# Performance work log

Measured on AMD Instinct MI355X. Metric: run time of the kernel, lower is better.

The kernel has to match this reference:

```python
import jax, jax.numpy as jnp
import numpy as np
import math

N_HEADS = 8
D_EMBED = 512
D_CROSS = 768
FF_DIM = 2048
D_HEAD = D_EMBED // N_HEADS


def _gelu_tanh(x):
    # matches the module's hand-written tanh GELU
    return 0.5 * x * (1.0 + jnp.tanh(jnp.sqrt(2.0 / jnp.pi) * (x + 0.044715 * x ** 3)))


def _layer_norm(x, g, b, eps=1e-5):
    mu = jnp.mean(x, axis=-1, keepdims=True)
    var = jnp.var(x, axis=-1, keepdims=True)
    return (x - mu) * jax.lax.rsqrt(var + eps) * g + b


def setup_inputs() -> dict:
    key = jax.random.key(0)
    ks = jax.random.split(key, 20)
    s = 0.02
    inp = {
        "x": jax.random.normal(ks[0], (2, 4096, D_EMBED), jnp.float32),
        "y": jax.random.normal(ks[1], (2, 77, D_CROSS), jnp.float32),
        # self-attention: fused in_proj [D, 3D]
        "sa_in_w": jax.random.normal(ks[2], (D_EMBED, 3 * D_EMBED), jnp.float32) * s,
        "sa_in_b": jnp.zeros((3 * D_EMBED,), jnp.float32),
        "sa_out_w": jax.random.normal(ks[3], (D_EMBED, D_EMBED), jnp.float32) * s,
        "sa_out_b": jnp.zeros((D_EMBED,), jnp.float32),
        # cross-attention
        "ca_q_w": jax.random.normal(ks[4], (D_EMBED, D_EMBED), jnp.float32) * s,
        "ca_q_b": jnp.zeros((D_EMBED,), jnp.float32),
        "ca_k_w": jax.random.normal(ks[5], (D_CROSS, D_EMBED), jnp.float32) * s,
        "ca_k_b": jnp.zeros((D_EMBED,), jnp.float32),
        "ca_v_w": jax.random.normal(ks[6], (D_CROSS, D_EMBED), jnp.float32) * s,
        "ca_v_b": jnp.zeros((D_EMBED,), jnp.float32),
        "ca_out_w": jax.random.normal(ks[7], (D_EMBED, D_EMBED), jnp.float32) * s,
        "ca_out_b": jnp.zeros((D_EMBED,), jnp.float32),
        # feed-forward
        "ff_w1": jax.random.normal(ks[8], (D_EMBED, FF_DIM), jnp.float32) * s,
        "ff_b1": jnp.zeros((FF_DIM,), jnp.float32),
        "ff_w2": jax.random.normal(ks[9], (FF_DIM, D_EMBED), jnp.float32) * s,
        "ff_b2": jnp.zeros((D_EMBED,), jnp.float32),
        # layer norms
        "ln1_g": jnp.ones((D_EMBED,), jnp.float32),
        "ln1_b": jnp.zeros((D_EMBED,), jnp.float32),
        "ln2_g": jnp.ones((D_EMBED,), jnp.float32),
        "ln2_b": jnp.zeros((D_EMBED,), jnp.float32),
        "ln3_g": jnp.ones((D_EMBED,), jnp.float32),
        "ln3_b": jnp.zeros((D_EMBED,), jnp.float32),
    }
    return inp


def _mha(q, k, v):
    # q,k,v: [B, S, D] -> split heads -> attention -> merge
    B, Sq, D = q.shape
    Skv = k.shape[1]
    qh = q.reshape(B, Sq, N_HEADS, D_HEAD).transpose(0, 2, 1, 3)
    kh = k.reshape(B, Skv, N_HEADS, D_HEAD).transpose(0, 2, 1, 3)
    vh = v.reshape(B, Skv, N_HEADS, D_HEAD).transpose(0, 2, 1, 3)
    scores = jnp.einsum("bhqd,bhkd->bhqk", qh, kh) / math.sqrt(D_HEAD)
    w = jax.nn.softmax(scores, axis=-1)
    out = jnp.einsum("bhqk,bhkd->bhqd", w, vh)
    return out.transpose(0, 2, 1, 3).reshape(B, Sq, D)


def reference(x, y, sa_in_w, sa_in_b, sa_out_w, sa_out_b,
              ca_q_w, ca_q_b, ca_k_w, ca_k_b, ca_v_w, ca_v_b, ca_out_w, ca_out_b,
              ff_w1, ff_b1, ff_w2, ff_b2,
              ln1_g, ln1_b, ln2_g, ln2_b, ln3_g, ln3_b):
    # self-attention (no causal mask; default causal_mask=False)
    qkv = x @ sa_in_w + sa_in_b
    q, k, v = jnp.split(qkv, 3, axis=-1)
    sa = _mha(q, k, v) @ sa_out_w + sa_out_b
    x = _layer_norm(x + sa, ln1_g, ln1_b)

    # cross-attention to y
    qc = x @ ca_q_w + ca_q_b
    kc = y @ ca_k_w + ca_k_b
    vc = y @ ca_v_w + ca_v_b
    ca = _mha(qc, kc, vc) @ ca_out_w + ca_out_b
    x = _layer_norm(x + ca, ln2_g, ln2_b)

    # feed-forward with tanh GELU
    ff = _gelu_tanh(x @ ff_w1 + ff_b1) @ ff_w2 + ff_b2
    x = _layer_norm(x + ff, ln3_g, ln3_b)
    return x
```

## Files before the change

kernel.cpp:

```cpp
#include <hip/hip_runtime.h>
#include <stdint.h>

typedef float floatx4 __attribute__((ext_vector_type(4)));
typedef __bf16 bf16x8 __attribute__((ext_vector_type(8)));
typedef unsigned int uintx4 __attribute__((ext_vector_type(4)));
typedef unsigned short ushort_t;

__device__ __forceinline__ float b2f(ushort_t u) {
  union { unsigned int i; float f; } x; x.i = ((unsigned int)u) << 16; return x.f;
}
__device__ __forceinline__ ushort_t f2b(float f) {
  union { float f; unsigned int i; } x; x.f = f;
  unsigned int i = x.i;
  return (ushort_t)((i + 0x7FFFu + ((i >> 16) & 1u)) >> 16);
}
__device__ __forceinline__ unsigned fbits(float f) {
  union { float f; unsigned u; } x; x.f = f; return x.u;
}
__device__ __forceinline__ uintx4 ld16(const void* p) {
  uintx4 v; __builtin_memcpy(&v, p, 16); return v;
}
__device__ __forceinline__ void st16(void* p, uintx4 v) { __builtin_memcpy(p, &v, 16); }
__device__ __forceinline__ floatx4 f4splat(float x) { floatx4 v = {x, x, x, x}; return v; }
__device__ __forceinline__ void sched_fence() { asm volatile("" ::: "memory"); }

__device__ __forceinline__ floatx4 mfma16(uintx4 a, uintx4 b, floatx4 c) {
  return __builtin_amdgcn_mfma_f32_16x16x32_bf16(
      __builtin_bit_cast(bf16x8, a), __builtin_bit_cast(bf16x8, b), c, 0, 0, 0);
}

__device__ __forceinline__ void gll16(const ushort_t* g, ushort_t* l) {
  __builtin_amdgcn_global_load_lds(
      (__attribute__((address_space(1))) void*)(g),
      (__attribute__((address_space(3))) void*)(l), 16, 0, 0);
}

template <int EPI, int NT>
__global__ __launch_bounds__(256, 2) void gemm_bt(
    const ushort_t* __restrict__ A, const ushort_t* __restrict__ Bt,
    const float* __restrict__ bias, void* __restrict__ Cout,
    int N, int K) {
  constexpr int NI = NT / 32;
  __shared__ alignas(16) ushort_t lA[128 * 32];
  __shared__ alignas(16) ushort_t lB[NT * 32];
  const int tid = threadIdx.x;
  const int wave = tid >> 6, lane = tid & 63;
  const int quad = lane >> 4, l16 = lane & 15;
  const int bm = blockIdx.y * 128, bn = blockIdx.x * NT;
  const int wm = (wave >> 1) * 64, wn = (wave & 1) * (NT / 2);

  const ushort_t* ag0 = A + (size_t)(bm + wave * 32 + (lane >> 2)) * K + (lane & 3) * 8;
  const ushort_t* ag1 = ag0 + (size_t)16 * K;
  ushort_t* la = lA + wave * 1024;
  const ushort_t* bg0;
  const ushort_t* bg1 = nullptr;
  ushort_t* lb;
  if (NT == 128) {
    bg0 = Bt + (size_t)(bn + wave * 32 + (lane >> 2)) * K + (lane & 3) * 8;
    bg1 = bg0 + (size_t)16 * K;
    lb = lB + wave * 1024;
  } else {
    bg0 = Bt + (size_t)(bn + wave * 16 + (lane >> 2)) * K + (lane & 3) * 8;
    lb = lB + wave * 512;
  }

  floatx4 acc[4][NI];
#pragma unroll
  for (int i = 0; i < 4; i++)
#pragma unroll
    for (int j = 0; j < NI; j++) acc[i][j] = f4splat(0.f);

  for (int k0 = 0; k0 < K; k0 += 32) {
    __syncthreads();
    gll16(ag0 + k0, la);
    gll16(ag1 + k0, la + 512);
    gll16(bg0 + k0, lb);
    if (NT == 128) gll16(bg1 + k0, lb + 512);
    __syncthreads();
    uintx4 af[4], bf[NI];
#pragma unroll
    for (int i = 0; i < 4; i++) af[i] = ld16(&lA[(wm + i * 16 + l16) * 32 + quad * 8]);
#pragma unroll
    for (int i = 0; i < NI; i++) bf[i] = ld16(&lB[(wn + i * 16 + l16) * 32 + quad * 8]);
#pragma unroll
    for (int mi = 0; mi < 4; mi++)
#pragma unroll
      for (int ni = 0; ni < NI; ni++) acc[mi][ni] = mfma16(af[mi], bf[ni], acc[mi][ni]);
  }

  float bv[NI];
#pragma unroll
  for (int ni = 0; ni < NI; ni++) bv[ni] = bias[bn + wn + ni * 16 + l16];

#pragma unroll
  for (int mi = 0; mi < 4; mi++)
#pragma unroll
    for (int ni = 0; ni < NI; ni++)
#pragma unroll
      for (int r = 0; r < 4; r++) {
        int row = bm + wm + mi * 16 + quad * 4 + r;
        int col = bn + wn + ni * 16 + l16;
        float v = acc[mi][ni][r] + bv[ni];
        if (EPI == 2) {
          float w = v + 0.044715f * v * v * v;
          float e = __builtin_amdgcn_exp2f(-2.3022084f * w);
          v = v * __builtin_amdgcn_rcpf(1.f + e);
        }
        if (EPI == 1)
          ((float*)Cout)[(size_t)row * N + col] = v;
        else
          ((ushort_t*)Cout)[(size_t)row * N + col] = f2b(v);
      }
}

__global__ __launch_bounds__(256) void pack_k(const ushort_t* __restrict__ qkv,
                                              ushort_t* __restrict__ KP) {
  int g = blockIdx.x * 256 + threadIdx.x;
  int lane = g & 63;
  int frag = (g >> 6) & 7;
  int kt = (g >> 9) & 63;
  int bh = g >> 15;
  int b = bh >> 3, h = bh & 7;
  int ni = frag >> 1, kf = frag & 1;
  int l16 = lane & 15, quad = lane >> 4;
  const ushort_t* src = qkv + (size_t)(b * 4096 + kt * 64 + ni * 16 + l16) * 1536 +
                        512 + h * 64 + kf * 32 + quad * 8;
  st16(KP + (size_t)g * 8, ld16(src));
}

__global__ __launch_bounds__(256) void pack_v(const ushort_t* __restrict__ qkv,
                                              ushort_t* __restrict__ VP) {
  __shared__ ushort_t t[64 * 72];
  int bh = blockIdx.x, kt = blockIdx.y;
  int b = bh >> 3, h = bh & 7;
  int tid = threadIdx.x;
#pragma unroll
  for (int i = 0; i < 2; i++) {
    int c = i * 256 + tid;
    int row = c >> 3, c8 = (c & 7) * 8;
    uintx4 d4 = ld16(qkv + (size_t)(b * 4096 + kt * 64 + row) * 1536 + 1024 + h * 64 + c8);
    ushort_t tmp[8];
    __builtin_memcpy(tmp, &d4, 16);
#pragma unroll
    for (int j = 0; j < 8; j++) t[(c8 + j) * 72 + row] = tmp[j];
  }
  __syncthreads();
#pragma unroll
  for (int i = 0; i < 2; i++) {
    int c = i * 256 + tid;
    int frag = c >> 6, lane = c & 63;
    int f = frag >> 2, dn = frag & 3;
    int l16 = lane & 15, quad = lane >> 4;
    uintx4 d4 = ld16(&t[(dn * 16 + l16) * 72 + f * 32 + quad * 8]);
    st16(VP + ((size_t)(bh * 64 + kt) * 8 + frag) * 512 + (size_t)lane * 8, d4);
  }
}

__global__ __launch_bounds__(256, 2) void flash_self(
    const ushort_t* __restrict__ qkv, const ushort_t* __restrict__ KP,
    const ushort_t* __restrict__ VP, ushort_t* __restrict__ outp) {
  __shared__ alignas(16) ushort_t lPT[4 * 32 * 72];
  const int tid = threadIdx.x, wave = tid >> 6, lane = tid & 63;
  const int quad = lane >> 4, l16 = lane & 15;
  const int bh = blockIdx.x, b = bh >> 3, h = bh & 7;
  const int qt = blockIdx.y;

  const ushort_t* Qb = qkv + (size_t)b * 4096 * 1536 + h * 64;
  const ushort_t* KPb = KP + (size_t)bh * 64 * 4096;
  const ushort_t* VPb = VP + (size_t)bh * 64 * 4096;

  uintx4 qf[2][2];
#pragma unroll
  for (int mi = 0; mi < 2; mi++)
#pragma unroll
    for (int kf = 0; kf < 2; kf++)
      qf[mi][kf] = ld16(Qb + (size_t)(qt * 128 + wave * 32 + mi * 16 + l16) * 1536 +
                        kf * 32 + quad * 8);

  floatx4 O[2][4];
#pragma unroll
  for (int mi = 0; mi < 2; mi++)
#pragma unroll
    for (int dn = 0; dn < 4; dn++) O[mi][dn] = f4splat(0.f);
  float lsum[2] = {0.f, 0.f};
  const float c = 0.18033688f;
  ushort_t* PTw = lPT + wave * 32 * 72;

#pragma unroll 2
  for (int kt = 0; kt < 64; kt++) {
    const ushort_t* kb = KPb + kt * 4096;
    uintx4 kfr[4][2];
#pragma unroll
    for (int ni = 0; ni < 4; ni++)
#pragma unroll
      for (int kf = 0; kf < 2; kf++)
        kfr[ni][kf] = ld16(kb + ((ni * 2 + kf) * 64 + lane) * 8);

    floatx4 S[2][4];
#pragma unroll
    for (int ni = 0; ni < 4; ni++)
#pragma unroll
      for (int mi = 0; mi < 2; mi++) {
        floatx4 z = f4splat(0.f);
        z = mfma16(kfr[ni][0], qf[mi][0], z);
        z = mfma16(kfr[ni][1], qf[mi][1], z);
        S[mi][ni] = z;
      }

    const ushort_t* vbp = VPb + kt * 4096;
    uintx4 vf[2][4];
#pragma unroll
    for (int f = 0; f < 2; f++)
#pragma unroll
      for (int dn = 0; dn < 4; dn++)
        vf[f][dn] = ld16(vbp + ((f * 4 + dn) * 64 + lane) * 8);

#pragma unroll
    for (int mi = 0; mi < 2; mi++) {
      float rs = 0.f;
#pragma unroll
      for (int ni = 0; ni < 4; ni++) {
        float p0 = __builtin_amdgcn_exp2f(S[mi][ni][0] * c);
        float p1 = __builtin_amdgcn_exp2f(S[mi][ni][1] * c);
        float p2 = __builtin_amdgcn_exp2f(S[mi][ni][2] * c);
        float p3 = __builtin_amdgcn_exp2f(S[mi][ni][3] * c);
        rs += (p0 + p1) + (p2 + p3);
        unsigned dd[2];
        dd[0] = (fbits(p1) & 0xFFFF0000u) | (fbits(p0) >> 16);
        dd[1] = (fbits(p3) & 0xFFFF0000u) | (fbits(p2) >> 16);
        __builtin_memcpy(&PTw[(mi * 16 + l16) * 72 + ni * 16 + quad * 4], dd, 8);
      }
      lsum[mi] += rs;
    }
    sched_fence();

#pragma unroll
    for (int f = 0; f < 2; f++) {
      uintx4 pf0 = ld16(&PTw[(0 + l16) * 72 + f * 32 + quad * 8]);
      uintx4 pf1 = ld16(&PTw[(16 + l16) * 72 + f * 32 + quad * 8]);
#pragma unroll
      for (int dn = 0; dn < 4; dn++) {
        O[0][dn] = mfma16(vf[f][dn], pf0, O[0][dn]);
        O[1][dn] = mfma16(vf[f][dn], pf1, O[1][dn]);
      }
    }
  }

#pragma unroll
  for (int mi = 0; mi < 2; mi++) {
    lsum[mi] += __shfl_xor(lsum[mi], 16);
    lsum[mi] += __shfl_xor(lsum[mi], 32);
  }

#pragma unroll
  for (int mi = 0; mi < 2; mi++) {
    float inv = 1.0f / lsum[mi];
    const size_t rowg = (size_t)b * 4096 + qt * 128 + wave * 32 + mi * 16 + l16;
#pragma unroll
    for (int dn = 0; dn < 4; dn++) {
      unsigned u0 = (unsigned)f2b(O[mi][dn][0] * inv) | ((unsigned)f2b(O[mi][dn][1] * inv) << 16);
      unsigned u1 = (unsigned)f2b(O[mi][dn][2] * inv) | ((unsigned)f2b(O[mi][dn][3] * inv) << 16);
      unsigned uu[2] = {u0, u1};
      __builtin_memcpy(outp + rowg * 512 + h * 64 + dn * 16 + quad * 4, uu, 8);
    }
  }
}

__global__ __launch_bounds__(256, 2) void cross_attn(
    const ushort_t* __restrict__ qc, const ushort_t* __restrict__ kc,
    const ushort_t* __restrict__ vc, ushort_t* __restrict__ outp) {
  __shared__ alignas(16) ushort_t lK[96 * 72];
  __shared__ alignas(16) ushort_t lV[64 * 104];
  __shared__ alignas(16) ushort_t lP[128 * 104];
  const int tid = threadIdx.x, wave = tid >> 6, lane = tid & 63;
  const int quad = lane >> 4, l16 = lane & 15;
  const int bh = blockIdx.y, b = bh >> 3, h = bh & 7;
  const int qt = blockIdx.x;

#pragma unroll
  for (int i = 0; i < 3; i++) {
    int ch = i * 256 + tid;
    int r = ch >> 3, c8 = ch & 7;
    uintx4 d = {0u, 0u, 0u, 0u};
    if (r < 77) d = ld16(kc + (size_t)(b * 77 + r) * 512 + h * 64 + c8 * 8);
    st16(&lK[r * 72 + c8 * 8], d);
  }
  for (int i = 0; i < 24; i++) {
    int e = i * 256 + tid;
    int dd = e / 96, s = e - dd * 96;
    ushort_t v = 0;
    if (s < 77) v = vc[(size_t)(b * 77 + s) * 512 + h * 64 + dd];
    lV[dd * 104 + s] = v;
  }
  __syncthreads();

  const int qr0 = qt * 128 + wave * 32;
  uintx4 qf[2][2];
#pragma unroll
  for (int mi = 0; mi < 2; mi++)
#pragma unroll
    for (int kf = 0; kf < 2; kf++)
      qf[mi][kf] =
          ld16(qc + (size_t)(b * 4096 + qr0 + mi * 16 + l16) * 512 + h * 64 + kf * 32 + quad * 8);

  floatx4 S[2][6];
#pragma unroll
  for (int ni = 0; ni < 6; ni++) {
    uintx4 k0 = ld16(&lK[(ni * 16 + l16) * 72 + quad * 8]);
    uintx4 k1 = ld16(&lK[(ni * 16 + l16) * 72 + 32 + quad * 8]);
#pragma unroll
    for (int mi = 0; mi < 2; mi++) {
      floatx4 z = f4splat(0.f);
      z = mfma16(qf[mi][0], k0, z);
      z = mfma16(qf[mi][1], k1, z);
      S[mi][ni] = z;
    }
  }
  const float c = 0.18033688f;
#pragma unroll
  for (int ni = 4; ni < 6; ni++)
    if (ni * 16 + l16 >= 77) {
      S[0][ni] = f4splat(-1e30f);
      S[1][ni] = f4splat(-1e30f);
    }

  floatx4 linv[2];
#pragma unroll
  for (int mi = 0; mi < 2; mi++) {
    floatx4 cm = S[mi][0];
#pragma unroll
    for (int ni = 1; ni < 6; ni++)
#pragma unroll
      for (int r = 0; r < 4; r++) cm[r] = fmaxf(cm[r], S[mi][ni][r]);
#pragma unroll
    for (int off = 1; off < 16; off <<= 1)
#pragma unroll
      for (int r = 0; r < 4; r++) cm[r] = fmaxf(cm[r], __shfl_xor(cm[r], off));
    floatx4 rs = f4splat(0.f);
#pragma unroll
    for (int ni = 0; ni < 6; ni++)
#pragma unroll
      for (int r = 0; r < 4; r++) {
        float p = __builtin_amdgcn_exp2f(S[mi][ni][r] * c - cm[r] * c);
        S[mi][ni][r] = p;
        rs[r] += p;
      }
#pragma unroll
    for (int off = 1; off < 16; off <<= 1)
#pragma unroll
      for (int r = 0; r < 4; r++) rs[r] += __shfl_xor(rs[r], off);
#pragma unroll
    for (int r = 0; r < 4; r++) linv[mi][r] = 1.0f / rs[r];
#pragma unroll
    for (int ni = 0; ni < 6; ni++)
#pragma unroll
      for (int r = 0; r < 4; r++)
        lP[(wave * 32 + mi * 16 + quad * 4 + r) * 104 + ni * 16 + l16] = f2b(S[mi][ni][r]);
  }
  sched_fence();

  floatx4 O[2][4];
#pragma unroll
  for (int mi = 0; mi < 2; mi++)
#pragma unroll
    for (int dn = 0; dn < 4; dn++) O[mi][dn] = f4splat(0.f);
#pragma unroll
  for (int kf = 0; kf < 3; kf++) {
    uintx4 pa0 = ld16(&lP[(wave * 32 + 0 + l16) * 104 + kf * 32 + quad * 8]);
    uintx4 pa1 = ld16(&lP[(wave * 32 + 16 + l16) * 104 + kf * 32 + quad * 8]);
#pragma unroll
    for (int dn = 0; dn < 4; dn++) {
      uintx4 vb = ld16(&lV[(dn * 16 + l16) * 104 + kf * 32 + quad * 8]);
      O[0][dn] = mfma16(pa0, vb, O[0][dn]);
      O[1][dn] = mfma16(pa1, vb, O[1][dn]);
    }
  }
#pragma unroll
  for (int mi = 0; mi < 2; mi++)
#pragma unroll
    for (int dn = 0; dn < 4; dn++)
#pragma unroll
      for (int r = 0; r < 4; r++) {
        int row = b * 4096 + qt * 128 + wave * 32 + mi * 16 + quad * 4 + r;
        int col = h * 64 + dn * 16 + l16;
        outp[(size_t)row * 512 + col] = f2b(O[mi][dn][r] * linv[mi][r]);
      }
}

template <int RESF>
__global__ __launch_bounds__(256) void ln_kernel(
    const float* __restrict__ p, const void* __restrict__ resv,
    const float* __restrict__ g, const float* __restrict__ bb,
    float* __restrict__ out32, ushort_t* __restrict__ outbf) {
  const int row = blockIdx.x * 4 + (threadIdx.x >> 6);
  const int lane = threadIdx.x & 63;
  const size_t base = (size_t)row * 512;
  float v[8];
  float s = 0.f, ss = 0.f;
#pragma unroll
  for (int i = 0; i < 2; i++) {
    int cidx = i * 256 + lane * 4;
    float4 pv; __builtin_memcpy(&pv, p + base + cidx, 16);
    float rv[4];
    if (RESF) {
      __builtin_memcpy(rv, (const float*)resv + base + cidx, 16);
    } else {
      ushort_t rr[4];
      __builtin_memcpy(rr, (const ushort_t*)resv + base + cidx, 8);
#pragma unroll
      for (int j = 0; j < 4; j++) rv[j] = b2f(rr[j]);
    }
    float pvv[4] = {pv.x, pv.y, pv.z, pv.w};
#pragma unroll
    for (int j = 0; j < 4; j++) {
      float a = pvv[j] + rv[j];
      v[i * 4 + j] = a;
      s += a;
      ss += a * a;
    }
  }
#pragma unroll
  for (int off = 1; off < 64; off <<= 1) {
    s += __shfl_xor(s, off);
    ss += __shfl_xor(ss, off);
  }
  float mean = s * (1.f / 512.f);
  float var = ss * (1.f / 512.f) - mean * mean;
  float rstd = rsqrtf(var + 1e-5f);
#pragma unroll
  for (int i = 0; i < 2; i++) {
    int cidx = i * 256 + lane * 4;
    float gv[4], bv2[4];
    __builtin_memcpy(gv, g + cidx, 16);
    __builtin_memcpy(bv2, bb + cidx, 16);
    float y[4];
#pragma unroll
    for (int j = 0; j < 4; j++) y[j] = (v[i * 4 + j] - mean) * rstd * gv[j] + bv2[j];
    if (out32) __builtin_memcpy(out32 + base + cidx, y, 16);
    if (outbf) {
      ushort_t o[4] = {f2b(y[0]), f2b(y[1]), f2b(y[2]), f2b(y[3])};
      __builtin_memcpy(outbf + base + cidx, o, 8);
    }
  }
}

__global__ __launch_bounds__(256) void small_gemm2(
    const float* __restrict__ y, const float* __restrict__ wk,
    const float* __restrict__ bk, const float* __restrict__ wv,
    const float* __restrict__ bv, ushort_t* __restrict__ kout,
    ushort_t* __restrict__ vout) {
  int bid = blockIdx.x;
  const float* W; const float* B; ushort_t* O;
  if (bid >= 308) { W = wv; B = bv; O = vout; bid -= 308; }
  else            { W = wk; B = bk; O = kout; }
  int idx = bid * 256 + threadIdx.x;
  if (idx >= 154 * 512) return;
  int r = idx >> 9, col = idx & 511;
  const float* ya = y + (size_t)r * 768;
  float acc = B[col];
#pragma unroll 4
  for (int k = 0; k < 768; k++) acc += ya[k] * W[(size_t)k * 512 + col];
  O[idx] = f2b(acc);
}

struct TransJob { const float* in; ushort_t* out; int ldi, ldo, nbx, start; };
struct TransJobs6 { TransJob j[6]; };

__global__ __launch_bounds__(256) void transpose6(TransJobs6 jobs) {
  __shared__ float t[32][33];
  int bid = blockIdx.x;
  int ji = 0;
#pragma unroll
  for (int i = 1; i < 6; i++)
    if (bid >= jobs.j[i].start) ji = i;
  TransJob J = jobs.j[ji];
  int local = bid - J.start;
  int by = local / J.nbx, bx = local - by * J.nbx;
  int r0 = by * 32, c0 = bx * 32;
  int tx = threadIdx.x & 31, ty = threadIdx.x >> 5;
#pragma unroll
  for (int i = 0; i < 4; i++)
    t[ty + 8 * i][tx] = J.in[(size_t)(r0 + ty + 8 * i) * J.ldi + c0 + tx];
  __syncthreads();
#pragma unroll
  for (int i = 0; i < 4; i++)
    J.out[(size_t)(c0 + ty + 8 * i) * J.ldo + r0 + tx] = f2b(t[tx][ty + 8 * i]);
}

__global__ __launch_bounds__(256) void xcvt(const float* __restrict__ in,
                                            ushort_t* __restrict__ out) {
  int i = (blockIdx.x * 256 + threadIdx.x) * 4;
  float4 v; __builtin_memcpy(&v, in + i, 16);
  ushort_t o[4] = {f2b(v.x), f2b(v.y), f2b(v.z), f2b(v.w)};
  __builtin_memcpy(out + i, o, 8);
}

extern "C" void kernel_launch(void* const* d_in, const int* in_sizes, int n_in,
                              void* d_out, int out_size, void* d_ws, size_t ws_size,
                              hipStream_t stream) {
  const size_t MiB = 1048576;
  if (ws_size < 64 * MiB) return;

  const float* x        = (const float*)d_in[0];
  const float* y        = (const float*)d_in[1];
  const float* sa_in_w  = (const float*)d_in[2];
  const float* sa_in_b  = (const float*)d_in[3];
  const float* sa_out_w = (const float*)d_in[4];
  const float* sa_out_b = (const float*)d_in[5];
  const float* ca_q_w   = (const float*)d_in[6];
  const float* ca_q_b   = (const float*)d_in[7];
  const float* ca_k_w   = (const float*)d_in[8];
  const float* ca_k_b   = (const float*)d_in[9];
  const float* ca_v_w   = (const float*)d_in[10];
  const float* ca_v_b   = (const float*)d_in[11];
  const float* ca_out_w = (const float*)d_in[12];
  const float* ca_out_b = (const float*)d_in[13];
  const float* ff_w1    = (const float*)d_in[14];
  const float* ff_b1    = (const float*)d_in[15];
  const float* ff_w2    = (const float*)d_in[16];
  const float* ff_b2    = (const float*)d_in[17];
  const float* ln1_g    = (const float*)d_in[18];
  const float* ln1_b    = (const float*)d_in[19];
  const float* ln2_g    = (const float*)d_in[20];
  const float* ln2_b    = (const float*)d_in[21];
  const float* ln3_g    = (const float*)d_in[22];
  const float* ln3_b    = (const float*)d_in[23];

  char* w = (char*)d_ws;
  ushort_t* QKV  = (ushort_t*)(w + 0);
  float*    P    = (float*)(w + 0);
  ushort_t* QC   = (ushort_t*)(w + 0);
  float*    P2   = (float*)(w + 0);
  ushort_t* FF   = (ushort_t*)(w + 0);
  ushort_t* ATT  = (ushort_t*)(w + 24 * MiB);
  ushort_t* KP   = (ushort_t*)(w + 32 * MiB);
  ushort_t* VP   = (ushort_t*)(w + 40 * MiB);
  float*    XB0  = (float*)(w + 32 * MiB);
  float*    P3   = (float*)(w + 32 * MiB);
  ushort_t* XBF  = (ushort_t*)(w + 48 * MiB);
  ushort_t* XB0b = (ushort_t*)(w + 48 * MiB);
  ushort_t* XB1b = (ushort_t*)(w + 48 * MiB);
  ushort_t* WT   = (ushort_t*)(w + 56 * MiB);
  ushort_t* KC   = (ushort_t*)(w + 63 * MiB);
  ushort_t* VC   = KC + 154 * 512;

  ushort_t* WT_sain  = WT;
  ushort_t* WT_saout = WT_sain + 786432;
  ushort_t* WT_caq   = WT_saout + 262144;
  ushort_t* WT_caout = WT_caq + 262144;
  ushort_t* WT_ff1   = WT_caout + 262144;
  ushort_t* WT_ff2   = WT_ff1 + 1048576;

  TransJobs6 tj;
  tj.j[0] = TransJob{sa_in_w,  WT_sain,  1536, 512, 48, 0};
  tj.j[1] = TransJob{sa_out_w, WT_saout, 512,  512, 16, 768};
  tj.j[2] = TransJob{ca_q_w,   WT_caq,   512,  512, 16, 1024};
  tj.j[3] = TransJob{ca_out_w, WT_caout, 512,  512, 16, 1280};
  tj.j[4] = TransJob{ff_w1,    WT_ff1,   2048, 512, 64, 1536};
  tj.j[5] = TransJob{ff_w2,    WT_ff2,   512, 2048, 16, 2560};
  transpose6<<<3584, 256, 0, stream>>>(tj);
  xcvt<<<4096, 256, 0, stream>>>(x, XBF);

  gemm_bt<0, 128><<<dim3(12, 64), 256, 0, stream>>>(XBF, WT_sain, sa_in_b, QKV, 1536, 512);
  pack_k<<<2048, 256, 0, stream>>>(QKV, KP);
  pack_v<<<dim3(16, 64), 256, 0, stream>>>(QKV, VP);
  flash_self<<<dim3(16, 32), 256, 0, stream>>>(QKV, KP, VP, ATT);
  gemm_bt<1, 64><<<dim3(8, 64), 256, 0, stream>>>(ATT, WT_saout, sa_out_b, P, 512, 512);
  ln_kernel<1><<<2048, 256, 0, stream>>>(P, x, ln1_g, ln1_b, XB0, XB0b);

  gemm_bt<0, 64><<<dim3(8, 64), 256, 0, stream>>>(XB0b, WT_caq, ca_q_b, QC, 512, 512);
  small_gemm2<<<616, 256, 0, stream>>>(y, ca_k_w, ca_k_b, ca_v_w, ca_v_b, KC, VC);
  cross_attn<<<dim3(32, 16), 256, 0, stream>>>(QC, KC, VC, ATT);
  gemm_bt<1, 64><<<dim3(8, 64), 256, 0, stream>>>(ATT, WT_caout, ca_out_b, P2, 512, 512);
  ln_kernel<1><<<2048, 256, 0, stream>>>(P2, XB0, ln2_g, ln2_b, nullptr, XB1b);

  gemm_bt<2, 128><<<dim3(16, 64), 256, 0, stream>>>(XB1b, WT_ff1, ff_b1, FF, 2048, 512);
  gemm_bt<1, 64><<<dim3(8, 64), 256, 0, stream>>>(FF, WT_ff2, ff_b2, P3, 512, 2048);
  ln_kernel<0><<<2048, 256, 0, stream>>>(P3, XB1b, ln3_g, ln3_b, (float*)d_out, nullptr);
}
```

Measured before the change: 441.3 us.

## Merge small prep kernels, store GEMM outputs in bf16, use packed bf16 convert

Combines the weight transpose and x conversion into one launch. Folds pack_k, pack_v and the cross-attention K/V projection into a single 'mid' kernel. Projection GEMMs now write bf16 instead of fp32 before the layer norms, and the second layer norm reads its residual in bf16 instead of fp32. Hardware packed bf16 conversion replaces the manual bit tricks where the builtin exists. The aim is fewer launches and less memory traffic, at the cost of lower precision in the residual path and the pre-LN sums.

```diff
diff --git a/kernel.cpp b/kernel.cpp
--- a/kernel.cpp
+++ b/kernel.cpp
@@ -17,6 +17,20 @@
 __device__ __forceinline__ unsigned fbits(float f) {
   union { float f; unsigned u; } x; x.f = f; return x.u;
 }
+__device__ __forceinline__ unsigned pk_rne(float a, float b) {
+#if __has_builtin(__builtin_amdgcn_cvt_pk_bf16_f32)
+  return __builtin_bit_cast(unsigned, __builtin_amdgcn_cvt_pk_bf16_f32(a, b));
+#else
+  return (unsigned)f2b(a) | ((unsigned)f2b(b) << 16);
+#endif
+}
+__device__ __forceinline__ unsigned pk_fast(float a, float b) {
+#if __has_builtin(__builtin_amdgcn_cvt_pk_bf16_f32)
+  return __builtin_bit_cast(unsigned, __builtin_amdgcn_cvt_pk_bf16_f32(a, b));
+#else
+  return (fbits(b) & 0xFFFF0000u) | (fbits(a) >> 16);
+#endif
+}
 __device__ __forceinline__ uintx4 ld16(const void* p) {
   uintx4 v; __builtin_memcpy(&v, p, 16); return v;
 }
@@ -38,7 +52,7 @@
 template <int EPI, int NT>
 __global__ __launch_bounds__(256, 2) void gemm_bt(
     const ushort_t* __restrict__ A, const ushort_t* __restrict__ Bt,
-    const float* __restrict__ bias, void* __restrict__ Cout,
+    const float* __restrict__ bias, ushort_t* __restrict__ Cout,
     int N, int K) {
   constexpr int NI = NT / 32;
   __shared__ alignas(16) ushort_t lA[128 * 32];
@@ -106,53 +120,100 @@
           float e = __builtin_amdgcn_exp2f(-2.3022084f * w);
           v = v * __builtin_amdgcn_rcpf(1.f + e);
         }
-        if (EPI == 1)
-          ((float*)Cout)[(size_t)row * N + col] = v;
-        else
-          ((ushort_t*)Cout)[(size_t)row * N + col] = f2b(v);
+        Cout[(size_t)row * N + col] = f2b(v);
       }
 }
 
-__global__ __launch_bounds__(256) void pack_k(const ushort_t* __restrict__ qkv,
-                                              ushort_t* __restrict__ KP) {
-  int g = blockIdx.x * 256 + threadIdx.x;
-  int lane = g & 63;
-  int frag = (g >> 6) & 7;
-  int kt = (g >> 9) & 63;
-  int bh = g >> 15;
-  int b = bh >> 3, h = bh & 7;
-  int ni = frag >> 1, kf = frag & 1;
-  int l16 = lane & 15, quad = lane >> 4;
-  const ushort_t* src = qkv + (size_t)(b * 4096 + kt * 64 + ni * 16 + l16) * 1536 +
-                        512 + h * 64 + kf * 32 + quad * 8;
-  st16(KP + (size_t)g * 8, ld16(src));
-}
-
-__global__ __launch_bounds__(256) void pack_v(const ushort_t* __restrict__ qkv,
-                                              ushort_t* __restrict__ VP) {
+struct TransJob { const float* in; ushort_t* out; int ldi, ldo, nbx, start; };
+struct TransJobs6 { TransJob j[6]; };
+
+__global__ __launch_bounds__(256) void prep(TransJobs6 jobs, const float* __restrict__ x,
+                                            ushort_t* __restrict__ xbf) {
+  __shared__ float t[32][33];
+  int bid = blockIdx.x;
+  if (bid >= 3584) {
+    int i = ((bid - 3584) * 256 + threadIdx.x) * 4;
+    float4 v; __builtin_memcpy(&v, x + i, 16);
+    unsigned o[2] = {pk_rne(v.x, v.y), pk_rne(v.z, v.w)};
+    __builtin_memcpy(xbf + i, o, 8);
+    return;
+  }
+  int ji = 0;
+#pragma unroll
+  for (int i = 1; i < 6; i++)
+    if (bid >= jobs.j[i].start) ji = i;
+  TransJob J = jobs.j[ji];
+  int local = bid - J.start;
+  int by = local / J.nbx, bx = local - by * J.nbx;
+  int r0 = by * 32, c0 = bx * 32;
+  int tx = threadIdx.x & 31, ty = threadIdx.x >> 5;
+#pragma unroll
+  for (int i = 0; i < 4; i++)
+    t[ty + 8 * i][tx] = J.in[(size_t)(r0 + ty + 8 * i) * J.ldi + c0 + tx];
+  __syncthreads();
+#pragma unroll
+  for (int i = 0; i < 4; i++)
+    J.out[(size_t)(c0 + ty + 8 * i) * J.ldo + r0 + tx] = f2b(t[tx][ty + 8 * i]);
+}
+
+__global__ __launch_bounds__(256) void mid(
+    const ushort_t* __restrict__ qkv, ushort_t* __restrict__ KP,
+    ushort_t* __restrict__ VP, const float* __restrict__ y,
+    const float* __restrict__ wk, const float* __restrict__ bk,
+    const float* __restrict__ wv, const float* __restrict__ bv,
+    ushort_t* __restrict__ kc, ushort_t* __restrict__ vc) {
   __shared__ ushort_t t[64 * 72];
-  int bh = blockIdx.x, kt = blockIdx.y;
-  int b = bh >> 3, h = bh & 7;
+  int bid = blockIdx.x;
   int tid = threadIdx.x;
-#pragma unroll
-  for (int i = 0; i < 2; i++) {
-    int c = i * 256 + tid;
-    int row = c >> 3, c8 = (c & 7) * 8;
-    uintx4 d4 = ld16(qkv + (size_t)(b * 4096 + kt * 64 + row) * 1536 + 1024 + h * 64 + c8);
-    ushort_t tmp[8];
-    __builtin_memcpy(tmp, &d4, 16);
-#pragma unroll
-    for (int j = 0; j < 8; j++) t[(c8 + j) * 72 + row] = tmp[j];
-  }
-  __syncthreads();
-#pragma unroll
-  for (int i = 0; i < 2; i++) {
-    int c = i * 256 + tid;
-    int frag = c >> 6, lane = c & 63;
-    int f = frag >> 2, dn = frag & 3;
+  if (bid < 2048) {
+    int g = bid * 256 + tid;
+    int lane = g & 63;
+    int frag = (g >> 6) & 7;
+    int kt = (g >> 9) & 63;
+    int bh = g >> 15;
+    int b = bh >> 3, h = bh & 7;
+    int ni = frag >> 1, kf = frag & 1;
     int l16 = lane & 15, quad = lane >> 4;
-    uintx4 d4 = ld16(&t[(dn * 16 + l16) * 72 + f * 32 + quad * 8]);
-    st16(VP + ((size_t)(bh * 64 + kt) * 8 + frag) * 512 + (size_t)lane * 8, d4);
+    const ushort_t* src = qkv + (size_t)(b * 4096 + kt * 64 + ni * 16 + l16) * 1536 +
+                          512 + h * 64 + kf * 32 + quad * 8;
+    st16(KP + (size_t)g * 8, ld16(src));
+  } else if (bid < 3072) {
+    int local = bid - 2048;
+    int bh = local >> 6, kt = local & 63;
+    int b = bh >> 3, h = bh & 7;
+#pragma unroll
+    for (int i = 0; i < 2; i++) {
+      int c = i * 256 + tid;
+      int row = c >> 3, c8 = (c & 7) * 8;
+      uintx4 d4 = ld16(qkv + (size_t)(b * 4096 + kt * 64 + row) * 1536 + 1024 + h * 64 + c8);
+      ushort_t tmp[8];
+      __builtin_memcpy(tmp, &d4, 16);
+#pragma unroll
+      for (int j = 0; j < 8; j++) t[(c8 + j) * 72 + row] = tmp[j];
+    }
+    __syncthreads();
+#pragma unroll
+    for (int i = 0; i < 2; i++) {
+      int c = i * 256 + tid;
+      int frag = c >> 6, lane = c & 63;
+      int f = frag >> 2, dn = frag & 3;
+      int l16 = lane & 15, quad = lane >> 4;
+      uintx4 d4 = ld16(&t[(dn * 16 + l16) * 72 + f * 32 + quad * 8]);
+      st16(VP + ((size_t)(bh * 64 + kt) * 8 + frag) * 512 + (size_t)lane * 8, d4);
+    }
+  } else {
+    int sb = bid - 3072;
+    const float* W; const float* B; ushort_t* O;
+    if (sb >= 308) { W = wv; B = bv; O = vc; sb -= 308; }
+    else           { W = wk; B = bk; O = kc; }
+    int idx = sb * 256 + tid;
+    if (idx >= 154 * 512) return;
+    int r = idx >> 9, col = idx & 511;
+    const float* ya = y + (size_t)r * 768;
+    float acc = B[col];
+#pragma unroll 4
+    for (int k = 0; k < 768; k++) acc += ya[k] * W[(size_t)k * 512 + col];
+    O[idx] = f2b(acc);
   }
 }
 
@@ -225,9 +286,7 @@
         float p2 = __builtin_amdgcn_exp2f(S[mi][ni][2] * c);
         float p3 = __builtin_amdgcn_exp2f(S[mi][ni][3] * c);
         rs += (p0 + p1) + (p2 + p3);
-        unsigned dd[2];
-        dd[0] = (fbits(p1) & 0xFFFF0000u) | (fbits(p0) >> 16);
-        dd[1] = (fbits(p3) & 0xFFFF0000u) | (fbits(p2) >> 16);
+        unsigned dd[2] = {pk_fast(p0, p1), pk_fast(p2, p3)};
         __builtin_memcpy(&PTw[(mi * 16 + l16) * 72 + ni * 16 + quad * 4], dd, 8);
       }
       lsum[mi] += rs;
@@ -258,9 +317,8 @@
     const size_t rowg = (size_t)b * 4096 + qt * 128 + wave * 32 + mi * 16 + l16;
 #pragma unroll
     for (int dn = 0; dn < 4; dn++) {
-      unsigned u0 = (unsigned)f2b(O[mi][dn][0] * inv) | ((unsigned)f2b(O[mi][dn][1] * inv) << 16);
-      unsigned u1 = (unsigned)f2b(O[mi][dn][2] * inv) | ((unsigned)f2b(O[mi][dn][3] * inv) << 16);
-      unsigned uu[2] = {u0, u1};
+      unsigned uu[2] = {pk_rne(O[mi][dn][0] * inv, O[mi][dn][1] * inv),
+                        pk_rne(O[mi][dn][2] * inv, O[mi][dn][3] * inv)};
       __builtin_memcpy(outp + rowg * 512 + h * 64 + dn * 16 + quad * 4, uu, 8);
     }
   }
@@ -389,7 +447,7 @@
 
 template <int RESF>
 __global__ __launch_bounds__(256) void ln_kernel(
-    const float* __restrict__ p, const void* __restrict__ resv,
+    const ushort_t* __restrict__ p, const void* __restrict__ resv,
     const float* __restrict__ g, const float* __restrict__ bb,
     float* __restrict__ out32, ushort_t* __restrict__ outbf) {
   const int row = blockIdx.x * 4 + (threadIdx.x >> 6);
@@ -400,7 +458,8 @@
 #pragma unroll
   for (int i = 0; i < 2; i++) {
     int cidx = i * 256 + lane * 4;
-    float4 pv; __builtin_memcpy(&pv, p + base + cidx, 16);
+    ushort_t pb[4];
+    __builtin_memcpy(pb, p + base + cidx, 8);
     float rv[4];
     if (RESF) {
       __builtin_memcpy(rv, (const float*)resv + base + cidx, 16);
@@ -410,10 +469,9 @@
 #pragma unroll
       for (int j = 0; j < 4; j++) rv[j] = b2f(rr[j]);
     }
-    float pvv[4] = {pv.x, pv.y, pv.z, pv.w};
 #pragma unroll
     for (int j = 0; j < 4; j++) {
-      float a = pvv[j] + rv[j];
+      float a = b2f(pb[j]) + rv[j];
       v[i * 4 + j] = a;
       s += a;
       ss += a * a;
@@ -438,61 +496,10 @@
     for (int j = 0; j < 4; j++) y[j] = (v[i * 4 + j] - mean) * rstd * gv[j] + bv2[j];
     if (out32) __builtin_memcpy(out32 + base + cidx, y, 16);
     if (outbf) {
-      ushort_t o[4] = {f2b(y[0]), f2b(y[1]), f2b(y[2]), f2b(y[3])};
+      unsigned o[2] = {pk_rne(y[0], y[1]), pk_rne(y[2], y[3])};
       __builtin_memcpy(outbf + base + cidx, o, 8);
     }
   }
-}
-
-__global__ __launch_bounds__(256) void small_gemm2(
-    const float* __restrict__ y, const float* __restrict__ wk,
-    const float* __restrict__ bk, const float* __restrict__ wv,
-    const float* __restrict__ bv, ushort_t* __restrict__ kout,
-    ushort_t* __restrict__ vout) {
-  int bid = blockIdx.x;
-  const float* W; const float* B; ushort_t* O;
-  if (bid >= 308) { W = wv; B = bv; O = vout; bid -= 308; }
-  else            { W = wk; B = bk; O = kout; }
-  int idx = bid * 256 + threadIdx.x;
-  if (idx >= 154 * 512) return;
-  int r = idx >> 9, col = idx & 511;
-  const float* ya = y + (size_t)r * 768;
-  float acc = B[col];
-#pragma unroll 4
-  for (int k = 0; k < 768; k++) acc += ya[k] * W[(size_t)k * 512 + col];
-  O[idx] = f2b(acc);
-}
-
-struct TransJob { const float* in; ushort_t* out; int ldi, ldo, nbx, start; };
-struct TransJobs6 { TransJob j[6]; };
-
-__global__ __launch_bounds__(256) void transpose6(TransJobs6 jobs) {
-  __shared__ float t[32][33];
-  int bid = blockIdx.x;
-  int ji = 0;
-#pragma unroll
-  for (int i = 1; i < 6; i++)
-    if (bid >= jobs.j[i].start) ji = i;
-  TransJob J = jobs.j[ji];
-  int local = bid - J.start;
-  int by = local / J.nbx, bx = local - by * J.nbx;
-  int r0 = by * 32, c0 = bx * 32;
-  int tx = threadIdx.x & 31, ty = threadIdx.x >> 5;
-#pragma unroll
-  for (int i = 0; i < 4; i++)
-    t[ty + 8 * i][tx] = J.in[(size_t)(r0 + ty + 8 * i) * J.ldi + c0 + tx];
-  __syncthreads();
-#pragma unroll
-  for (int i = 0; i < 4; i++)
-    J.out[(size_t)(c0 + ty + 8 * i) * J.ldo + r0 + tx] = f2b(t[tx][ty + 8 * i]);
-}
-
-__global__ __launch_bounds__(256) void xcvt(const float* __restrict__ in,
-                                            ushort_t* __restrict__ out) {
-  int i = (blockIdx.x * 256 + threadIdx.x) * 4;
-  float4 v; __builtin_memcpy(&v, in + i, 16);
-  ushort_t o[4] = {f2b(v.x), f2b(v.y), f2b(v.z), f2b(v.w)};
-  __builtin_memcpy(out + i, o, 8);
 }
 
 extern "C" void kernel_launch(void* const* d_in, const int* in_sizes, int n_in,
@@ -528,18 +535,15 @@
 
   char* w = (char*)d_ws;
   ushort_t* QKV  = (ushort_t*)(w + 0);
-  float*    P    = (float*)(w + 0);
   ushort_t* QC   = (ushort_t*)(w + 0);
-  float*    P2   = (float*)(w + 0);
   ushort_t* FF   = (ushort_t*)(w + 0);
   ushort_t* ATT  = (ushort_t*)(w + 24 * MiB);
+  ushort_t* XBF  = (ushort_t*)(w + 32 * MiB);
   ushort_t* KP   = (ushort_t*)(w + 32 * MiB);
+  ushort_t* XB0b = (ushort_t*)(w + 32 * MiB);
   ushort_t* VP   = (ushort_t*)(w + 40 * MiB);
-  float*    XB0  = (float*)(w + 32 * MiB);
-  float*    P3   = (float*)(w + 32 * MiB);
-  ushort_t* XBF  = (ushort_t*)(w + 48 * MiB);
-  ushort_t* XB0b = (ushort_t*)(w + 48 * MiB);
-  ushort_t* XB1b = (ushort_t*)(w + 48 * MiB);
+  ushort_t* XB1b = (ushort_t*)(w + 40 * MiB);
+  ushort_t* P    = (ushort_t*)(w + 48 * MiB);
   ushort_t* WT   = (ushort_t*)(w + 56 * MiB);
   ushort_t* KC   = (ushort_t*)(w + 63 * MiB);
   ushort_t* VC   = KC + 154 * 512;
@@ -558,23 +562,20 @@
   tj.j[3] = TransJob{ca_out_w, WT_caout, 512,  512, 16, 1280};
   tj.j[4] = TransJob{ff_w1,    WT_ff1,   2048, 512, 64, 1536};
   tj.j[5] = TransJob{ff_w2,    WT_ff2,   512, 2048, 16, 2560};
-  transpose6<<<3584, 256, 0, stream>>>(tj);
-  xcvt<<<4096, 256, 0, stream>>>(x, XBF);
+  prep<<<7680, 256, 0, stream>>>(tj, x, XBF);
 
   gemm_bt<0, 128><<<dim3(12, 64), 256, 0, stream>>>(XBF, WT_sain, sa_in_b, QKV, 1536, 512);
-  pack_k<<<2048, 256, 0, stream>>>(QKV, KP);
-  pack_v<<<dim3(16, 64), 256, 0, stream>>>(QKV, VP);
+  mid<<<3688, 256, 0, stream>>>(QKV, KP, VP, y, ca_k_w, ca_k_b, ca_v_w, ca_v_b, KC, VC);
   flash_self<<<dim3(16, 32), 256, 0, stream>>>(QKV, KP, VP, ATT);
-  gemm_bt<1, 64><<<dim3(8, 64), 256, 0, stream>>>(ATT, WT_saout, sa_out_b, P, 512, 512);
-  ln_kernel<1><<<2048, 256, 0, stream>>>(P, x, ln1_g, ln1_b, XB0, XB0b);
+  gemm_bt<0, 64><<<dim3(8, 64), 256, 0, stream>>>(ATT, WT_saout, sa_out_b, P, 512, 512);
+  ln_kernel<1><<<2048, 256, 0, stream>>>(P, x, ln1_g, ln1_b, nullptr, XB0b);
 
   gemm_bt<0, 64><<<dim3(8, 64), 256, 0, stream>>>(XB0b, WT_caq, ca_q_b, QC, 512, 512);
-  small_gemm2<<<616, 256, 0, stream>>>(y, ca_k_w, ca_k_b, ca_v_w, ca_v_b, KC, VC);
   cross_attn<<<dim3(32, 16), 256, 0, stream>>>(QC, KC, VC, ATT);
-  gemm_bt<1, 64><<<dim3(8, 64), 256, 0, stream>>>(ATT, WT_caout, ca_out_b, P2, 512, 512);
-  ln_kernel<1><<<2048, 256, 0, stream>>>(P2, XB0, ln2_g, ln2_b, nullptr, XB1b);
+  gemm_bt<0, 64><<<dim3(8, 64), 256, 0, stream>>>(ATT, WT_caout, ca_out_b, P, 512, 512);
+  ln_kernel<0><<<2048, 256, 0, stream>>>(P, XB0b, ln2_g, ln2_b, nullptr, XB1b);
 
   gemm_bt<2, 128><<<dim3(16, 64), 256, 0, stream>>>(XB1b, WT_ff1, ff_b1, FF, 2048, 512);
-  gemm_bt<1, 64><<<dim3(8, 64), 256, 0, stream>>>(FF, WT_ff2, ff_b2, P3, 512, 2048);
-  ln_kernel<0><<<2048, 256, 0, stream>>>(P3, XB1b, ln3_g, ln3_b, (float*)d_out, nullptr);
-}
+  gemm_bt<0, 64><<<dim3(8, 64), 256, 0, stream>>>(FF, WT_ff2, ff_b2, P, 512, 2048);
+  ln_kernel<0><<<2048, 256, 0, stream>>>(P, XB1b, ln3_g, ln3_b, (float*)d_out, nullptr);
+}
```

Measured after the change: 425.5 us. 1.04x faster.
